# Kernel optimization log

Hardware: AMD Instinct MI355X
Metric: run time of the kernel (lower is better)

## Reference

```python
import jax, jax.numpy as jnp
import numpy as np

DIM = 1024
HEADS = 16
DH = 64          # dim_for_head
INNER = HEADS * DH
SCALE = DH ** -0.5


def setup_inputs() -> dict:
    key = jax.random.key(0)
    ks = jax.random.split(key, 5)
    x = jax.random.normal(ks[0], (4, 2048, DIM), dtype=jnp.float32)
    ln_gamma = jnp.ones((DIM,), dtype=jnp.float32)
    ln_beta = jnp.zeros((DIM,), dtype=jnp.float32)
    # torch Linear weight is [out, in]; store same layout, apply as x @ W.T
    w_qkv = jax.random.normal(ks[1], (3 * INNER, DIM), dtype=jnp.float32) * (DIM ** -0.5)
    w_out = jax.random.normal(ks[2], (DIM, INNER), dtype=jnp.float32) * (INNER ** -0.5)
    b_out = jnp.zeros((DIM,), dtype=jnp.float32)
    return {"x": x, "ln_gamma": ln_gamma, "ln_beta": ln_beta,
            "w_qkv": w_qkv, "w_out": w_out, "b_out": b_out}


def reference(x, ln_gamma, ln_beta, w_qkv, w_out, b_out):
    b, n, d = x.shape
    # LayerNorm (eps=1e-5 as torch default)
    mu = jnp.mean(x, axis=-1, keepdims=True)
    var = jnp.mean(jnp.square(x - mu), axis=-1, keepdims=True)
    xn = (x - mu) * jax.lax.rsqrt(var + 1e-5) * ln_gamma + ln_beta
    # QKV projection
    qkv = xn @ w_qkv.T                                   # [b, n, 3*inner]
    q, k, v = jnp.split(qkv, 3, axis=-1)
    reshape = lambda t: t.reshape(b, n, HEADS, DH).transpose(0, 2, 1, 3)  # [b, h, n, d]
    q, k, v = reshape(q), reshape(k), reshape(v)
    # Attention
    dots = jnp.einsum('bhqd,bhkd->bhqk', q, k) * SCALE
    attn = jax.nn.softmax(dots, axis=-1)                 # dropout p=0 -> identity
    out = jnp.einsum('bhqk,bhkd->bhqd', attn, v)
    out = out.transpose(0, 2, 1, 3).reshape(b, n, INNER)
    return out @ w_out.T + b_out
```

## Files before the change

### kernel.cpp

```cpp
#include <hip/hip_runtime.h>
#include <stdint.h>


typedef __attribute__((ext_vector_type(4)))  float  f32x4;
typedef __attribute__((ext_vector_type(16))) float  f32x16;
typedef __attribute__((ext_vector_type(8)))  short  s16x8;
typedef __attribute__((ext_vector_type(4)))  unsigned short u16x4;
typedef __attribute__((ext_vector_type(2)))  int    i32x2;
typedef __attribute__((ext_vector_type(4)))  int    i32x4;

__device__ __forceinline__ float bf2f(short b) {
    union { unsigned u; float f; } x; x.u = ((unsigned)(unsigned short)b) << 16; return x.f;
}
__device__ __forceinline__ short f2bf(float f) {
    union { float f; unsigned u; } x; x.f = f;
    unsigned r = x.u + 0x7fffu + ((x.u >> 16) & 1u);
    return (short)(r >> 16);
}
__device__ __forceinline__ float exp2_hw(float x) {
    float r; asm("v_exp_f32 %0, %1" : "=v"(r) : "v"(x)); return r;
}

__device__ __forceinline__ void gload_lds16(const void* g, void* l) {
    __builtin_amdgcn_global_load_lds(
        (const __attribute__((address_space(1))) void*)g,
        (__attribute__((address_space(3))) void*)l, 16, 0, 0);
}

__global__ __launch_bounds__(256)
void prep_kernel(const float* __restrict__ x, const float* __restrict__ gamma,
                 const float* __restrict__ beta, short* __restrict__ xn,
                 const float* __restrict__ wqkv, const float* __restrict__ wout,
                 short* __restrict__ wqkvb, short* __restrict__ woutb) {
    if (blockIdx.x < 2048) {
        const int w = threadIdx.x >> 6, l = threadIdx.x & 63;
        const size_t row = (size_t)blockIdx.x * 4 + w;
        const float* xr = x + row * 1024;
        f32x4 v[4];
        float sum = 0.f, ss = 0.f;
#pragma unroll
        for (int i = 0; i < 4; i++) {
            v[i] = *(const f32x4*)(xr + (l + 64 * i) * 4);
#pragma unroll
            for (int e = 0; e < 4; e++) { sum += v[i][e]; ss += v[i][e] * v[i][e]; }
        }
#pragma unroll
        for (int d = 1; d < 64; d <<= 1) { sum += __shfl_xor(sum, d); ss += __shfl_xor(ss, d); }
        const float mu   = sum * (1.f / 1024.f);
        const float var  = ss * (1.f / 1024.f) - mu * mu;
        const float rstd = rsqrtf(var + 1e-5f);
#pragma unroll
        for (int i = 0; i < 4; i++) {
            f32x4 g  = *(const f32x4*)(gamma + (l + 64 * i) * 4);
            f32x4 bt = *(const f32x4*)(beta  + (l + 64 * i) * 4);
            u16x4 o;
#pragma unroll
            for (int e = 0; e < 4; e++)
                o[e] = (unsigned short)f2bf((v[i][e] - mu) * rstd * g[e] + bt[e]);
            *(u16x4*)(xn + row * 1024 + (l + 64 * i) * 4) = o;
        }
    } else {
        int i = (blockIdx.x - 2048) * blockDim.x + threadIdx.x;
        const float* in; short* out; float sc = 1.0f;
        if (i < 786432) {
            in = wqkv; out = wqkvb;
            if ((i >> 8) < 1024) sc = 0.18033688011112042f;
        } else {
            i -= 786432; in = wout; out = woutb;
        }
        f32x4 v = ((const f32x4*)in)[i];
        u16x4 o;
        o.x = (unsigned short)f2bf(v.x * sc); o.y = (unsigned short)f2bf(v.y * sc);
        o.z = (unsigned short)f2bf(v.z * sc); o.w = (unsigned short)f2bf(v.w * sc);
        ((u16x4*)out)[i] = o;
    }
}

template <int NX, int NJ, int MODE, int MAP>
__global__ __launch_bounds__(512, 2)
void gemm256(const short* __restrict__ A, const short* __restrict__ W,
             short* __restrict__ outb, float* __restrict__ outf,
             const float* __restrict__ bias, short* __restrict__ vt,
             int M, int N, int K) {
    extern __shared__ short smem[];
    short* Albuf = smem;
    short* Blbuf = smem + 32768;
    const int tid = threadIdx.x;
    const int w = tid >> 6, l = tid & 63;
    const int wr = w >> 2, wc = w & 3;
    const int nb = gridDim.x, bid = blockIdx.x;
    int m0, n0;
    if constexpr (MAP == 1) {
        const int x = bid & 7, s = bid >> 3;
        const int sg = s >> 4, off = s & 15;
        m0 = (x * 4 + (off >> 2)) * 256;
        n0 = (sg * 4 + (off & 3)) * (NJ * 64);
    } else {
        const int swz = (bid & 7) * (nb >> 3) + (bid >> 3);
        m0 = (swz / NX) * 256; n0 = (swz % NX) * (NJ * 64);
    }
    const int lx = l & 15, hi4 = l >> 4, l7 = l & 7;
    const int srow = l >> 3;
    const int scs  = (l & 7) ^ srow;

    f32x4 acc[8][NJ];
#pragma unroll
    for (int i = 0; i < 8; i++)
#pragma unroll
        for (int j = 0; j < NJ; j++) acc[i][j] = (f32x4)0.f;

    auto STAGE = [&](int buf, int t) {
        const int k0 = t * 64;
#pragma unroll
        for (int p = 0; p < 4; p++) {
            const int row = p * 64 + w * 8 + srow;
            gload_lds16(A + (size_t)(m0 + row) * K + k0 + scs * 8,
                        Albuf + buf * 16384 + (p * 64 + w * 8) * 64);
        }
#pragma unroll
        for (int p = 0; p < NJ; p++) {
            const int row = p * 64 + w * 8 + srow;
            gload_lds16(W + (size_t)(n0 + row) * K + k0 + scs * 8,
                        Blbuf + buf * (NJ * 4096) + (p * 64 + w * 8) * 64);
        }
    };

    STAGE(0, 0);
    const int NT = K >> 6;
    for (int t = 0; t < NT; ++t) {
        const int cur = t & 1;
        if (t + 1 < NT) {
            STAGE(cur ^ 1, t + 1);
            if constexpr (NJ == 3) asm volatile("s_waitcnt vmcnt(7)" ::: "memory");
            else                   asm volatile("s_waitcnt vmcnt(6)" ::: "memory");
        } else {
            asm volatile("s_waitcnt vmcnt(0)" ::: "memory");
        }
        __builtin_amdgcn_s_barrier();
        const short* Ab = Albuf + cur * 16384;
        const short* Bb = Blbuf + cur * (NJ * 4096);

        s16x8 bfr[2][NJ];
#pragma unroll
        for (int kc = 0; kc < 2; kc++)
#pragma unroll
            for (int j = 0; j < NJ; j++) {
                const int R = wc * (NJ * 16) + j * 16 + lx;
                bfr[kc][j] = *(const s16x8*)(Bb + R * 64 + (((kc * 4 + hi4) ^ l7) * 8));
            }

#pragma unroll
        for (int p = 0; p < 2; p++) {
            s16x8 afr[4][2];
#pragma unroll
            for (int ii = 0; ii < 4; ii++)
#pragma unroll
                for (int kc = 0; kc < 2; kc++) {
                    const int R = wr * 128 + (p * 4 + ii) * 16 + lx;
                    afr[ii][kc] = *(const s16x8*)(Ab + R * 64 + (((kc * 4 + hi4) ^ l7) * 8));
                }
            __builtin_amdgcn_s_barrier();
            __builtin_amdgcn_s_setprio(1);
#pragma unroll
            for (int kc = 0; kc < 2; kc++)
#pragma unroll
                for (int ii = 0; ii < 4; ii++)
#pragma unroll
                    for (int j = 0; j < NJ; j++)
                        acc[p * 4 + ii][j] = __builtin_amdgcn_mfma_f32_16x16x32_bf16(
                            afr[ii][kc], bfr[kc][j], acc[p * 4 + ii][j], 0, 0, 0);
            __builtin_amdgcn_s_setprio(0);
            __builtin_amdgcn_s_barrier();
        }
    }

    const int lr = hi4 * 4;
#pragma unroll
    for (int i = 0; i < 8; i++) {
        const int rb = m0 + wr * 128 + i * 16 + lr;
#pragma unroll
        for (int j = 0; j < NJ; j++) {
            const int ccb = n0 + wc * (NJ * 16) + j * 16;
            const int cc = ccb + lx;
            if (MODE == 2 && ccb >= 2048) {
                const int hh = (cc - 2048) >> 6, dd = (cc - 2048) & 63;
                const int bI = rb >> 11, seq = rb & 2047;
                u16x4 o;
#pragma unroll
                for (int r = 0; r < 4; r++) o[r] = (unsigned short)f2bf(acc[i][j][r]);
                *(u16x4*)(vt + ((size_t)(bI * 16 + hh) * 64 + dd) * 2048 + seq) = o;
            } else {
                const float bv = (MODE == 1) ? bias[cc] : 0.f;
#pragma unroll
                for (int r = 0; r < 4; r++) {
                    if (MODE == 1) outf[(size_t)(rb + r) * N + cc] = acc[i][j][r] + bv;
                    else           outb[(size_t)(rb + r) * N + cc] = f2bf(acc[i][j][r]);
                }
            }
        }
    }
}

__global__ __launch_bounds__(256, 2)
void attn_kernel(const short* __restrict__ qkv, const short* __restrict__ vtg,
                 short* __restrict__ aout) {
    __shared__ short KV[2][2][64 * 64];
    const int tid = threadIdx.x, w = tid >> 6, l = tid & 63;
    const int bid = blockIdx.x;
    const int swz = (bid & 7) * 64 + (bid >> 3);
    const int qt = swz & 7, bh = swz >> 3;
    const int b = bh >> 4, h = bh & 15;
    const int q0 = qt * 256;
    const int y = l & 31, hi = l >> 5, l7 = l & 7;
    const short* Qp  = qkv + (size_t)b * 2048 * 3072 + h * 64;
    const short* Kp  = Qp + 1024;
    const short* Vtp = vtg + (size_t)bh * 64 * 2048;

    s16x8 bq[2][4];
#pragma unroll
    for (int u = 0; u < 2; u++) {
        const int qrow = q0 + w * 64 + u * 32 + y;
#pragma unroll
        for (int kc = 0; kc < 4; kc++)
            bq[u][kc] = *(const s16x8*)(Qp + (size_t)qrow * 3072 + kc * 16 + hi * 8);
    }

    f32x16 oc[2][2], ls[2];
#pragma unroll
    for (int u = 0; u < 2; u++) { oc[u][0] = (f32x16)0.f; oc[u][1] = (f32x16)0.f; ls[u] = (f32x16)0.f; }

    s16x8 ones;
#pragma unroll
    for (int e = 0; e < 8; e++) ones[e] = (short)0x3F80;

    const int srow = l >> 3;
    const int scs  = (l & 7) ^ srow;
    auto stage = [&](int par, int kv) {
#pragma unroll
        for (int p = 0; p < 2; p++) {
            const int row = w * 16 + p * 8 + srow;
            gload_lds16(Kp  + (size_t)(kv + row) * 3072 + scs * 8, &KV[par][0][(w * 16 + p * 8) * 64]);
            gload_lds16(Vtp + (size_t)row * 2048 + kv + scs * 8,   &KV[par][1][(w * 16 + p * 8) * 64]);
        }
    };

    const int Abase = y * 64 + ((hi ^ (l7 & 1)) * 8);
    int cofs[4];
#pragma unroll
    for (int j = 0; j < 4; j++) cofs[j] = ((l7 >> 1) ^ j) * 16;

    auto tilestep = [&](int par, int kv) {
        __syncthreads();
        if (kv + 64 < 2048) stage(par ^ 1, kv + 64);
        const short* Kb = &KV[par][0][0];
        const short* Vb = &KV[par][1][0];

        f32x16 s[2][2];
        s[0][0] = (f32x16)0.f; s[0][1] = (f32x16)0.f;
        s[1][0] = (f32x16)0.f; s[1][1] = (f32x16)0.f;
        __builtin_amdgcn_s_setprio(1);
#pragma unroll
        for (int kc = 0; kc < 4; kc++) {
#pragma unroll
            for (int kb = 0; kb < 2; kb++) {
                s16x8 ak = *(const s16x8*)(Kb + kb * 2048 + Abase + cofs[kc]);
                s[0][kb] = __builtin_amdgcn_mfma_f32_32x32x16_bf16(ak, bq[0][kc], s[0][kb], 0, 0, 0);
                s[1][kb] = __builtin_amdgcn_mfma_f32_32x32x16_bf16(ak, bq[1][kc], s[1][kb], 0, 0, 0);
            }
        }
        __builtin_amdgcn_s_setprio(0);

        int W0[2][2][8];
#pragma unroll
        for (int u = 0; u < 2; u++) {
#pragma unroll
            for (int kb = 0; kb < 2; kb++)
#pragma unroll
                for (int r = 0; r < 16; r++) s[u][kb][r] = exp2_hw(s[u][kb][r]);
#pragma unroll
            for (int kb = 0; kb < 2; kb++)
#pragma unroll
                for (int i = 0; i < 8; i++)
                    asm("v_cvt_pk_bf16_f32 %0, %1, %2"
                        : "=v"(W0[u][kb][i]) : "v"(s[u][kb][2 * i]), "v"(s[u][kb][2 * i + 1]));
        }

        __builtin_amdgcn_s_setprio(1);
#pragma unroll
        for (int a = 0; a < 2; a++)
#pragma unroll
            for (int bb = 0; bb < 2; bb++) {
                const int st = a * 2 + bb;
                s16x8 bv0 = *(const s16x8*)(Vb + 0 * 2048 + Abase + cofs[st]);
                s16x8 bv1 = *(const s16x8*)(Vb + 1 * 2048 + Abase + cofs[st]);
#pragma unroll
                for (int u = 0; u < 2; u++) {
                    i32x2 r0 = __builtin_amdgcn_permlane32_swap(W0[u][a][4 * bb + 0], W0[u][a][4 * bb + 2], false, false);
                    i32x2 r1 = __builtin_amdgcn_permlane32_swap(W0[u][a][4 * bb + 1], W0[u][a][4 * bb + 3], false, false);
                    union { i32x4 wv; s16x8 hv; } uu;
                    uu.wv = (i32x4){r0.x, r1.x, r0.y, r1.y};
                    ls[u]    = __builtin_amdgcn_mfma_f32_32x32x16_bf16(uu.hv, ones, ls[u], 0, 0, 0);
                    oc[u][0] = __builtin_amdgcn_mfma_f32_32x32x16_bf16(uu.hv, bv0, oc[u][0], 0, 0, 0);
                    oc[u][1] = __builtin_amdgcn_mfma_f32_32x32x16_bf16(uu.hv, bv1, oc[u][1], 0, 0, 0);
                }
            }
        __builtin_amdgcn_s_setprio(0);
    };

    stage(0, 0);
    for (int kv = 0; kv < 2048; kv += 128) {
        tilestep(0, kv);
        tilestep(1, kv + 64);
    }

#pragma unroll
    for (int u = 0; u < 2; u++)
#pragma unroll
        for (int r = 0; r < 16; r++) {
            const int qrr = (r & 3) + 8 * (r >> 2) + 4 * hi;
            const float ivr = 1.f / ls[u][r];
            const size_t row = (size_t)b * 2048 + q0 + w * 64 + u * 32 + qrr;
#pragma unroll
            for (int t2 = 0; t2 < 2; t2++)
                aout[row * 1024 + h * 64 + t2 * 32 + y] = f2bf(oc[u][t2][r] * ivr);
        }
}

extern "C" void kernel_launch(void* const* d_in, const int* in_sizes, int n_in,
                              void* d_out, int out_size, void* d_ws, size_t ws_size,
                              hipStream_t stream) {
    const float* x    = (const float*)d_in[0];
    const float* g    = (const float*)d_in[1];
    const float* be   = (const float*)d_in[2];
    const float* wqkv = (const float*)d_in[3];
    const float* wout = (const float*)d_in[4];
    const float* bo   = (const float*)d_in[5];
    float* out = (float*)d_out;

    char* ws = (char*)d_ws;
    short* xn    = (short*)(ws);
    short* wqkvb = (short*)(ws + 16777216);
    short* woutb = (short*)(ws + 16777216 + 6291456);
    short* qkvb  = (short*)(ws + 25165824);
    short* vtg   = (short*)(ws + 75497472);
    short* attb  = xn;

    (void)hipFuncSetAttribute((const void*)gemm256<16, 3, 2, 1>,
                              hipFuncAttributeMaxDynamicSharedMemorySize, 114688);
    (void)hipFuncSetAttribute((const void*)gemm256<8, 2, 1, 0>,
                              hipFuncAttributeMaxDynamicSharedMemorySize, 98304);

    prep_kernel<<<dim3(6144), 256, 0, stream>>>(x, g, be, xn, wqkv, wout, wqkvb, woutb);
    gemm256<16, 3, 2, 1><<<dim3(512), 512, 114688, stream>>>(xn, wqkvb, qkvb, nullptr, nullptr, vtg, 8192, 3072, 1024);
    attn_kernel<<<dim3(512), 256, 0, stream>>>(qkvb, vtg, attb);
    gemm256<8, 2, 1, 0><<<dim3(256), 512, 98304, stream>>>(attb, woutb, nullptr, out, bo, nullptr, 8192, 1024, 1024);
}
```

Baseline: 170.8 us.

## Read K and V tiles directly from global memory instead of LDS staging

Removes the double-buffered LDS staging of K and V tiles, along with its per-tile barrier and swizzled addressing. Each wave now loads its MFMA operands for K and the transposed V directly from global memory every iteration. This drops the synchronization and the LDS footprint, which could raise occupancy. In exchange, the four waves in a block no longer share the tile, so each one fetches it separately through the caches, and there is no prefetch to hide global load latency.

```diff
diff --git a/kernel.cpp b/kernel.cpp
--- a/kernel.cpp
+++ b/kernel.cpp
@@ -204,14 +204,13 @@
 __global__ __launch_bounds__(256, 2)
 void attn_kernel(const short* __restrict__ qkv, const short* __restrict__ vtg,
                  short* __restrict__ aout) {
-    __shared__ short KV[2][2][64 * 64];
     const int tid = threadIdx.x, w = tid >> 6, l = tid & 63;
     const int bid = blockIdx.x;
     const int swz = (bid & 7) * 64 + (bid >> 3);
     const int qt = swz & 7, bh = swz >> 3;
     const int b = bh >> 4, h = bh & 15;
     const int q0 = qt * 256;
-    const int y = l & 31, hi = l >> 5, l7 = l & 7;
+    const int y = l & 31, hi = l >> 5;
     const short* Qp  = qkv + (size_t)b * 2048 * 3072 + h * 64;
     const short* Kp  = Qp + 1024;
     const short* Vtp = vtg + (size_t)bh * 64 * 2048;
@@ -233,28 +232,10 @@
 #pragma unroll
     for (int e = 0; e < 8; e++) ones[e] = (short)0x3F80;
 
-    const int srow = l >> 3;
-    const int scs  = (l & 7) ^ srow;
-    auto stage = [&](int par, int kv) {
-#pragma unroll
-        for (int p = 0; p < 2; p++) {
-            const int row = w * 16 + p * 8 + srow;
-            gload_lds16(Kp  + (size_t)(kv + row) * 3072 + scs * 8, &KV[par][0][(w * 16 + p * 8) * 64]);
-            gload_lds16(Vtp + (size_t)row * 2048 + kv + scs * 8,   &KV[par][1][(w * 16 + p * 8) * 64]);
-        }
-    };
-
-    const int Abase = y * 64 + ((hi ^ (l7 & 1)) * 8);
-    int cofs[4];
-#pragma unroll
-    for (int j = 0; j < 4; j++) cofs[j] = ((l7 >> 1) ^ j) * 16;
-
-    auto tilestep = [&](int par, int kv) {
-        __syncthreads();
-        if (kv + 64 < 2048) stage(par ^ 1, kv + 64);
-        const short* Kb = &KV[par][0][0];
-        const short* Vb = &KV[par][1][0];
-
+    const short* Krow = Kp  + (size_t)y * 3072 + hi * 8;
+    const short* Vrow = Vtp + (size_t)y * 2048 + hi * 8;
+
+    for (int kv = 0; kv < 2048; kv += 64) {
         f32x16 s[2][2];
         s[0][0] = (f32x16)0.f; s[0][1] = (f32x16)0.f;
         s[1][0] = (f32x16)0.f; s[1][1] = (f32x16)0.f;
@@ -263,7 +244,7 @@
         for (int kc = 0; kc < 4; kc++) {
 #pragma unroll
             for (int kb = 0; kb < 2; kb++) {
-                s16x8 ak = *(const s16x8*)(Kb + kb * 2048 + Abase + cofs[kc]);
+                s16x8 ak = *(const s16x8*)(Krow + (size_t)(kv + kb * 32) * 3072 + kc * 16);
                 s[0][kb] = __builtin_amdgcn_mfma_f32_32x32x16_bf16(ak, bq[0][kc], s[0][kb], 0, 0, 0);
                 s[1][kb] = __builtin_amdgcn_mfma_f32_32x32x16_bf16(ak, bq[1][kc], s[1][kb], 0, 0, 0);
             }
@@ -291,8 +272,8 @@
 #pragma unroll
             for (int bb = 0; bb < 2; bb++) {
                 const int st = a * 2 + bb;
-                s16x8 bv0 = *(const s16x8*)(Vb + 0 * 2048 + Abase + cofs[st]);
-                s16x8 bv1 = *(const s16x8*)(Vb + 1 * 2048 + Abase + cofs[st]);
+                s16x8 bv0 = *(const s16x8*)(Vrow + (size_t)(0 * 32) * 2048 + kv + st * 16);
+                s16x8 bv1 = *(const s16x8*)(Vrow + (size_t)(1 * 32) * 2048 + kv + st * 16);
 #pragma unroll
                 for (int u = 0; u < 2; u++) {
                     i32x2 r0 = __builtin_amdgcn_permlane32_swap(W0[u][a][4 * bb + 0], W0[u][a][4 * bb + 2], false, false);
@@ -305,12 +286,6 @@
                 }
             }
         __builtin_amdgcn_s_setprio(0);
-    };
-
-    stage(0, 0);
-    for (int kv = 0; kv < 2048; kv += 128) {
-        tilestep(0, kv);
-        tilestep(1, kv + 64);
     }
 
 #pragma unroll
```

Measured after the change: 224.4 us. 31.4% more time.
